# Performance work log

Hardware: AMD Instinct MI355X
Metric: run time of the kernel (lower is better)

The kernel has to match this reference:

```python
import jax, jax.numpy as jnp
import numpy as np

HEADS = 16
DIM_HEAD = 64
QUERY_DIM = 1024
CONTEXT_DIM = 1024
D_ATTN = HEADS * DIM_HEAD
SCALE = DIM_HEAD ** -0.5


def setup_inputs() -> dict:
    key = jax.random.key(0)
    ks = jax.random.split(key, 7)
    B, N, M = 4, 2048, 1024
    x = jax.random.normal(ks[0], (B, N, QUERY_DIM), dtype=jnp.float32)
    context = jax.random.normal(ks[1], (B, M, CONTEXT_DIM), dtype=jnp.float32)
    # Linear weights stored as [in, out] (no bias for Q/K/V, bias for to_out)
    s = 0.02
    Wq = jax.random.normal(ks[2], (QUERY_DIM, D_ATTN), dtype=jnp.float32) * s
    Wk = jax.random.normal(ks[3], (CONTEXT_DIM, D_ATTN), dtype=jnp.float32) * s
    Wv = jax.random.normal(ks[4], (CONTEXT_DIM, D_ATTN), dtype=jnp.float32) * s
    Wo = jax.random.normal(ks[5], (D_ATTN, QUERY_DIM), dtype=jnp.float32) * s
    bo = jax.random.normal(ks[6], (QUERY_DIM,), dtype=jnp.float32) * s
    return {"x": x, "context": context, "Wq": Wq, "Wk": Wk, "Wv": Wv, "Wo": Wo, "bo": bo}


def reference(x, context, Wq, Wk, Wv, Wo, bo):
    B, N, _ = x.shape
    M = context.shape[1]
    Q = (x @ Wq).reshape(B, N, HEADS, DIM_HEAD)        # b n h d
    K = (context @ Wk).reshape(B, M, HEADS, DIM_HEAD)  # b m h d
    V = (context @ Wv).reshape(B, M, HEADS, DIM_HEAD)
    # scores: b q h m  (matches torch einsum 'bqhd,bhmd->bqhm')
    scores = jnp.einsum('bqhd,bmhd->bqhm', Q, K) * SCALE
    attn = jax.nn.softmax(scores, axis=-1)
    out = jnp.einsum('bqhm,bmhd->bqhd', attn, V)
    out = out.reshape(B, N, D_ATTN)
    return out @ Wo + bo  # dropout p=0.0 -> identity
```

## Files before the change

### kernel.cpp

```cpp
#include <hip/hip_runtime.h>
#include <math.h>


#define HEADS 16
#define DHEAD 64
#define DM    1024
#define BQ    4
#define NQ    2048
#define MK    1024

typedef unsigned short u16;
typedef __attribute__((ext_vector_type(8))) short bf16x8;
typedef __attribute__((ext_vector_type(4))) float f32x4;
typedef __attribute__((ext_vector_type(16))) float f32x16;

__device__ __forceinline__ u16 f2bf(float f) {
  unsigned u = __builtin_bit_cast(unsigned, f);
  u = u + 0x7FFFu + ((u >> 16) & 1u);
  return (u16)(u >> 16);
}

__device__ __forceinline__ unsigned cvtpk(float lo, float hi2) {
  unsigned r;
  asm("v_cvt_pk_bf16_f32 %0, %1, %2" : "=v"(r) : "v"(lo), "v"(hi2));
  return r;
}

__device__ __forceinline__ float max3f(float a, float b, float c) {
  float d;
  asm("v_max3_f32 %0, %1, %2, %3" : "=v"(d) : "v"(a), "v"(b), "v"(c));
  return d;
}

__device__ __forceinline__ void gld16(const u16* g, u16* l) {
  __builtin_amdgcn_global_load_lds((const __attribute__((address_space(1))) void*)g,
                                   (__attribute__((address_space(3))) void*)l,
                                   16, 0, 0);
}

__global__ void k_cvt(const float* __restrict__ in, u16* __restrict__ out, int n8) {
  int i = blockIdx.x * 256 + threadIdx.x;
  if (i >= n8) return;
  float4 a = ((const float4*)in)[i * 2];
  float4 b = ((const float4*)in)[i * 2 + 1];
  union { u16 h[8]; int4 v; } r;
  r.h[0] = f2bf(a.x); r.h[1] = f2bf(a.y); r.h[2] = f2bf(a.z); r.h[3] = f2bf(a.w);
  r.h[4] = f2bf(b.x); r.h[5] = f2bf(b.y); r.h[6] = f2bf(b.z); r.h[7] = f2bf(b.w);
  ((int4*)out)[i] = r.v;
}

__global__ void k_wt(const float* __restrict__ W0, const float* __restrict__ W1,
                     const float* __restrict__ W2, const float* __restrict__ W3,
                     u16* __restrict__ out) {
  __shared__ float t[32][33];
  const float* W = blockIdx.z == 0 ? W0 : blockIdx.z == 1 ? W1 : blockIdx.z == 2 ? W2 : W3;
  u16* o = out + (size_t)blockIdx.z * DM * DM;
  int r0 = blockIdx.y * 32, c0 = blockIdx.x * 32;
  int tx = threadIdx.x, ty = threadIdx.y;
  for (int i = ty; i < 32; i += 8) t[i][tx] = W[(size_t)(r0 + i) * DM + c0 + tx];
  __syncthreads();
  for (int i = ty; i < 32; i += 8) o[(size_t)(c0 + i) * DM + r0 + tx] = f2bf(t[tx][i]);
}


#define VM6 asm volatile("s_waitcnt vmcnt(6)" ::: "memory")

#define STAGE_A8(bufi, h, kof) do {                                          \
  gld16(gA + (size_t)(h) * 131072 + (kof), &As8[bufi][(h) * 8192 + w * 512]); \
  gld16(gA + (size_t)(h) * 131072 + 65536 + (kof),                           \
        &As8[bufi][(h) * 8192 + 4096 + w * 512]);                            \
} while (0)

#define STAGE_B8(bufi, h, kof) do {                                          \
  gld16(gB + (size_t)(h) * 131072 + (kof), &Bs8[bufi][(h) * 8192 + w * 512]); \
  gld16(gB + (size_t)(h) * 131072 + 65536 + (kof),                           \
        &Bs8[bufi][(h) * 8192 + 4096 + w * 512]);                            \
} while (0)

#define RD_A8(qm) do { _Pragma("unroll")                                     \
  for (int mi = 0; mi < 4; ++mi) {                                           \
    const u16* pa = &As8[cur][((qm) * 128 + wmo + mi * 16 + lrow) * 64];     \
    af8[mi][0] = *(const bf16x8*)(pa + fo0);                                 \
    af8[mi][1] = *(const bf16x8*)(pa + (fo0 ^ 32));                          \
  } } while (0)

#define RD_B8(qn) do { _Pragma("unroll")                                     \
  for (int ni = 0; ni < 2; ++ni) {                                           \
    const u16* pb = &Bs8[cur][((qn) * 128 + wno + ni * 16 + lrow) * 64];     \
    bf8[ni][0] = *(const bf16x8*)(pb + fo0);                                 \
    bf8[ni][1] = *(const bf16x8*)(pb + (fo0 ^ 32));                          \
  } } while (0)

#define MM16(qm, qn) do {                                                    \
  __builtin_amdgcn_s_setprio(1);                                             \
  _Pragma("unroll")                                                          \
  for (int mi = 0; mi < 4; ++mi)                                             \
    _Pragma("unroll")                                                        \
    for (int ni = 0; ni < 2; ++ni) {                                         \
      acc[qm][qn][mi][ni] = __builtin_amdgcn_mfma_f32_16x16x32_bf16(         \
          af8[mi][0], bf8[ni][0], acc[qm][qn][mi][ni], 0, 0, 0);             \
      acc[qm][qn][mi][ni] = __builtin_amdgcn_mfma_f32_16x16x32_bf16(         \
          af8[mi][1], bf8[ni][1], acc[qm][qn][mi][ni], 0, 0, 0);             \
    }                                                                        \
  __builtin_amdgcn_s_setprio(0);                                             \
} while (0)

#define PH8(RDS, STG, VM, qm, qn) do {                                       \
  RDS;                                                                       \
  __builtin_amdgcn_sched_barrier(0);                                         \
  STG;                                                                       \
  VM;                                                                        \
  __builtin_amdgcn_s_barrier();                                              \
  asm volatile("s_waitcnt lgkmcnt(0)" ::: "memory");                         \
  __builtin_amdgcn_sched_barrier(0);                                         \
  MM16(qm, qn);                                                              \
  __builtin_amdgcn_sched_barrier(0);                                         \
  __builtin_amdgcn_s_barrier();                                              \
} while (0)

__global__ __launch_bounds__(512, 2) void k_gemm_qkv(const u16* __restrict__ xb,
                                                     const u16* __restrict__ cb,
                                                     const u16* __restrict__ wt,
                                                     u16* __restrict__ Qb,
                                                     u16* __restrict__ Kb,
                                                     u16* __restrict__ Vtb) {
  __shared__ u16 As8[2][16384];
  __shared__ u16 Bs8[2][16384];
  int lin = blockIdx.x;
  int swz = (lin & 7) * 32 + (lin >> 3);
  int p = swz >> 2, bx = swz & 3;
  const u16* A; const u16* Bt; u16* obf; int row0, mode;
  if (p < 32)      { A = xb; Bt = wt;           obf = Qb;  row0 = p * 256;        mode = 0; }
  else if (p < 48) { A = cb; Bt = wt + 1048576; obf = Kb;  row0 = (p - 32) * 256; mode = 0; }
  else             { A = cb; Bt = wt + 2097152; obf = Vtb; row0 = (p - 48) * 256; mode = 1; }
  int col0 = bx * 256;
  int t = threadIdx.x;
  int w = t >> 6, lane = t & 63, lrow = lane & 15, lgrp = lane >> 4;
  int wmo = (w >> 2) * 64, wno = (w & 3) * 32;
  int fo0 = (lgrp ^ (lrow & 7)) * 8;
  f32x4 acc[2][2][4][2] = {};
  bf16x8 af8[4][2], bf8[2][2];
  int srow = t >> 3, sunit = (t & 7) ^ ((t >> 3) & 7);
  const u16* gA = A  + (size_t)(row0 + srow) * DM + sunit * 8;
  const u16* gB = Bt + (size_t)(col0 + srow) * DM + sunit * 8;

  STAGE_A8(0, 0, 0);
  STAGE_B8(0, 1, 0);
  STAGE_B8(0, 0, 0);
  STAGE_A8(0, 1, 0);
  STAGE_A8(1, 0, 64);
  STAGE_B8(1, 1, 64);
  VM6;
  __syncthreads();

  #pragma unroll 2
  for (int u = 0; u < 16; ++u) {
    int cur = u & 1, nxt = cur ^ 1;
    int k1 = (u >= 15 ? 15 : u + 1) * 64;
    int k2 = (u >= 14 ? 15 : u + 2) * 64;
    PH8({ RD_A8(0); RD_B8(0); }, STAGE_B8(nxt, 0, k1), VM6,     0, 0);
    PH8({ RD_B8(1); },           STAGE_A8(nxt, 1, k1), (void)0, 0, 1);
    PH8({ RD_A8(1); },           STAGE_A8(cur, 0, k2), (void)0, 1, 1);
    PH8({ RD_B8(0); },           STAGE_B8(cur, 1, k2), VM6,     1, 0);
  }

  #pragma unroll
  for (int qm = 0; qm < 2; ++qm)
    #pragma unroll
    for (int qn = 0; qn < 2; ++qn)
      #pragma unroll
      for (int mi = 0; mi < 4; ++mi)
        #pragma unroll
        for (int ni = 0; ni < 2; ++ni)
          #pragma unroll
          for (int j = 0; j < 4; ++j) {
            int gr = row0 + qm * 128 + wmo + mi * 16 + lgrp * 4 + j;
            int gc = col0 + qn * 128 + wno + ni * 16 + lrow;
            float v = acc[qm][qn][mi][ni][j];
            if (mode == 0) {
              obf[(size_t)gr * DM + gc] = f2bf(v);
            } else {
              int b = gr >> 10, m = gr & 1023;
              obf[((size_t)(b * DM + gc)) * MK + m] = f2bf(v);
            }
          }
}

#define OSTG_A(bufi, h, kof) do {                                            \
  gld16(gA + (size_t)(h) * 131072 + (kof), &As8[bufi][(h) * 8192 + w * 512]); \
  gld16(gA + (size_t)(h) * 131072 + 65536 + (kof),                           \
        &As8[bufi][(h) * 8192 + 4096 + w * 512]);                            \
} while (0)

#define OSTG_B(bufi, h, kof)                                                 \
  gld16(gB + (size_t)(h) * 65536 + (kof), &Bs8[bufi][(h) * 4096 + w * 512])

#define ORD_A(qm) do { _Pragma("unroll")                                     \
  for (int mi = 0; mi < 2; ++mi) {                                           \
    const u16* pa = &As8[cur][((qm) * 128 + wmo + mi * 16 + lrow) * 64];     \
    af[mi][0] = *(const bf16x8*)(pa + fo0);                                  \
    af[mi][1] = *(const bf16x8*)(pa + (fo0 ^ 32));                           \
  } } while (0)

#define ORD_B(qn, dst) do { _Pragma("unroll")                                \
  for (int ni = 0; ni < 2; ++ni) {                                           \
    const u16* pb = &Bs8[cur][((qn) * 64 + wno + ni * 16 + lrow) * 64];      \
    dst[ni][0] = *(const bf16x8*)(pb + fo0);                                 \
    dst[ni][1] = *(const bf16x8*)(pb + (fo0 ^ 32));                          \
  } } while (0)

#define OMM(qm, qn, bfq) do {                                                \
  __builtin_amdgcn_s_setprio(1);                                             \
  _Pragma("unroll")                                                          \
  for (int mi = 0; mi < 2; ++mi)                                             \
    _Pragma("unroll")                                                        \
    for (int ni = 0; ni < 2; ++ni) {                                         \
      acc[qm][qn][mi][ni] = __builtin_amdgcn_mfma_f32_16x16x32_bf16(         \
          af[mi][0], bfq[ni][0], acc[qm][qn][mi][ni], 0, 0, 0);              \
      acc[qm][qn][mi][ni] = __builtin_amdgcn_mfma_f32_16x16x32_bf16(         \
          af[mi][1], bfq[ni][1], acc[qm][qn][mi][ni], 0, 0, 0);              \
    }                                                                        \
  __builtin_amdgcn_s_setprio(0);                                             \
} while (0)

#define OPH(RDS, STG, VM, qm, qn, bfq) do {                                  \
  RDS;                                                                       \
  __builtin_amdgcn_sched_barrier(0);                                         \
  STG;                                                                       \
  VM;                                                                        \
  __builtin_amdgcn_s_barrier();                                              \
  asm volatile("s_waitcnt lgkmcnt(0)" ::: "memory");                         \
  __builtin_amdgcn_sched_barrier(0);                                         \
  OMM(qm, qn, bfq);                                                          \
  __builtin_amdgcn_sched_barrier(0);                                         \
  __builtin_amdgcn_s_barrier();                                              \
} while (0)

__global__ __launch_bounds__(512, 2) void k_gemm_o(const u16* __restrict__ A,
                                                   const u16* __restrict__ Bt,
                                                   float* __restrict__ of32,
                                                   const float* __restrict__ bias) {
  __shared__ u16 As8[2][16384];
  __shared__ u16 Bs8[2][8192];
  int lin = blockIdx.x;
  int swz = (lin & 7) * 32 + (lin >> 3);
  int p = swz >> 3, bx = swz & 7;
  int row0 = p * 256, col0 = bx * 128;
  int t = threadIdx.x;
  int w = t >> 6, lane = t & 63, lrow = lane & 15, lgrp = lane >> 4;
  int wmo = (w >> 1) * 32, wno = (w & 1) * 32;
  int fo0 = (lgrp ^ (lrow & 7)) * 8;
  f32x4 acc[2][2][2][2] = {};
  bf16x8 af[2][2], bfA[2][2], bfB[2][2];
  int srow = t >> 3, sunit = (t & 7) ^ ((t >> 3) & 7);
  const u16* gA = A  + (size_t)(row0 + srow) * DM + sunit * 8;
  const u16* gB = Bt + (size_t)(col0 + srow) * DM + sunit * 8;

  OSTG_A(0, 0, 0);
  OSTG_B(0, 1, 0);
  OSTG_B(0, 0, 0);
  OSTG_A(0, 1, 0);
  OSTG_A(1, 0, 64);
  OSTG_B(1, 1, 64);
  asm volatile("s_waitcnt vmcnt(5)" ::: "memory");
  __syncthreads();

  #pragma unroll 2
  for (int u = 0; u < 16; ++u) {
    int cur = u & 1, nxt = cur ^ 1;
    int k1 = (u >= 15 ? 15 : u + 1) * 64;
    int k2 = (u >= 14 ? 15 : u + 2) * 64;
    OPH({ ORD_A(0); ORD_B(0, bfA); }, OSTG_B(nxt, 0, k1),
        asm volatile("s_waitcnt vmcnt(4)" ::: "memory"), 0, 0, bfA);
    OPH({ ORD_B(1, bfB); },           OSTG_A(nxt, 1, k1), (void)0, 0, 1, bfB);
    OPH({ ORD_A(1); },                OSTG_A(cur, 0, k2), (void)0, 1, 1, bfB);
    OPH({ (void)0; },                 OSTG_B(cur, 1, k2),
        asm volatile("s_waitcnt vmcnt(5)" ::: "memory"), 1, 0, bfA);
  }

  #pragma unroll
  for (int qm = 0; qm < 2; ++qm)
    #pragma unroll
    for (int qn = 0; qn < 2; ++qn)
      #pragma unroll
      for (int mi = 0; mi < 2; ++mi)
        #pragma unroll
        for (int ni = 0; ni < 2; ++ni)
          #pragma unroll
          for (int j = 0; j < 4; ++j) {
            int gr = row0 + qm * 128 + wmo + mi * 16 + lgrp * 4 + j;
            int gc = col0 + qn * 64 + wno + ni * 16 + lrow;
            of32[(size_t)gr * DM + gc] = acc[qm][qn][mi][ni][j] + bias[gc];
          }
}

#define BUILD_PFRAG(sv, base, frag) {                     \
  unsigned a_ = cvtpk(sv[base + 0], sv[base + 1]);        \
  unsigned c_ = cvtpk(sv[base + 2], sv[base + 3]);        \
  unsigned b_ = cvtpk(sv[base + 4], sv[base + 5]);        \
  unsigned d_ = cvtpk(sv[base + 6], sv[base + 7]);        \
  asm("v_permlane32_swap_b32 %0, %1" : "+v"(a_), "+v"(b_)); \
  asm("v_permlane32_swap_b32 %0, %1" : "+v"(c_), "+v"(d_)); \
  union { unsigned w[4]; bf16x8 v; } u_;                  \
  u_.w[0] = a_;  u_.w[1] = c_;                            \
  u_.w[2] = b_;  u_.w[3] = d_;                            \
  frag = u_.v; }

#define PV_CHUNK(sv, base, c) {                                               \
  bf16x8 pf_; BUILD_PFRAG(sv, base, pf_);                                     \
  int mo_ = ((c) * 16 + hi * 8) ^ sw;                                         \
  bf16x8 vf0_ = *(const bf16x8*)&Vl[cur][ln * 64 + mo_];                      \
  bf16x8 vf1_ = *(const bf16x8*)&Vl[cur][(32 + ln) * 64 + mo_];               \
  __builtin_amdgcn_s_setprio(1);                                              \
  o0 = __builtin_amdgcn_mfma_f32_32x32x16_bf16(vf0_, pf_, o0, 0, 0, 0);       \
  o1 = __builtin_amdgcn_mfma_f32_32x32x16_bf16(vf1_, pf_, o1, 0, 0, 0);       \
  __builtin_amdgcn_s_setprio(0); }

__device__ __forceinline__ float max16(const f32x16 &v) {
  float m0 = max3f(v[0], v[1], v[2]);
  float m1 = max3f(v[3], v[4], v[5]);
  float m2 = max3f(v[6], v[7], v[8]);
  float m3 = max3f(v[9], v[10], v[11]);
  float m4 = max3f(v[12], v[13], v[14]);
  float a = max3f(m0, m1, m2);
  float b = max3f(m3, m4, v[15]);
  return fmaxf(a, b);
}

__device__ __forceinline__ float sum16(const f32x16 &v) {
  float a = (v[0] + v[1]) + (v[2] + v[3]);
  float b = (v[4] + v[5]) + (v[6] + v[7]);
  float c = (v[8] + v[9]) + (v[10] + v[11]);
  float d = (v[12] + v[13]) + (v[14] + v[15]);
  return (a + b) + (c + d);
}

__global__ __launch_bounds__(512) void k_attn(const u16* __restrict__ Q,
                                              const u16* __restrict__ K,
                                              const u16* __restrict__ Vt,
                                              u16* __restrict__ O) {
  __shared__ __align__(16) u16 Kl[2][4096];
  __shared__ __align__(16) u16 Vl[2][4096];
  int wgid = blockIdx.x;
  int bh = (wgid & 7) * 8 + (wgid >> 6);
  int nt = (wgid >> 3) & 7;
  int b = bh >> 4, h = bh & 15;
  int n0 = nt * 256;
  int t = threadIdx.x, w = t >> 6, lane = t & 63;
  int ln = lane & 31, hi = lane >> 5;
  const float s2 = 0.18033688011112042f;

  int qrow = n0 + w * 32 + ln;
  const u16* qp = &Q[(((size_t)(b * NQ + qrow)) * HEADS + h) * DHEAD + hi * 8];
  bf16x8 qf0 = *(const bf16x8*)(qp);
  bf16x8 qf1 = *(const bf16x8*)(qp + 16);
  bf16x8 qf2 = *(const bf16x8*)(qp + 32);
  bf16x8 qf3 = *(const bf16x8*)(qp + 48);

  f32x16 o0 = {}, o1 = {};
  float M_ = -1e30f, L_ = 0.f;

  int srow = t >> 3, sp = (t & 7) * 8;
  const u16* kg = &K[(((size_t)(b * MK + srow)) * HEADS + h) * DHEAD + sp];
  const u16* vg = &Vt[((size_t)(b * DM) + h * DHEAD + srow) * MK + sp];
  int sd = srow * 64 + (sp ^ ((srow & 7) << 3));
  int sw = (ln & 7) << 3;

  int4 kv = *(const int4*)kg;
  int4 vv = *(const int4*)vg;
  *(int4*)&Kl[0][sd] = kv;
  *(int4*)&Vl[0][sd] = vv;
  __syncthreads();

  for (int it = 0; it < 16; ++it) {
    int cur = it & 1;
    if (it < 15) {
      kv = *(const int4*)(kg + (size_t)(it + 1) * (64 * HEADS * DHEAD));
      vv = *(const int4*)(vg + (it + 1) * 64);
    }

    f32x16 s0 = {}, s1 = {};
    __builtin_amdgcn_s_setprio(1);
    #pragma unroll
    for (int kd = 0; kd < 4; ++kd) {
      int doff = (kd * 16 + hi * 8) ^ sw;
      bf16x8 kf0 = *(const bf16x8*)&Kl[cur][ln * 64 + doff];
      bf16x8 kf1 = *(const bf16x8*)&Kl[cur][(32 + ln) * 64 + doff];
      bf16x8 qk = kd == 0 ? qf0 : kd == 1 ? qf1 : kd == 2 ? qf2 : qf3;
      s0 = __builtin_amdgcn_mfma_f32_32x32x16_bf16(kf0, qk, s0, 0, 0, 0);
      s1 = __builtin_amdgcn_mfma_f32_32x32x16_bf16(kf1, qk, s1, 0, 0, 0);
    }
    __builtin_amdgcn_s_setprio(0);

    float vm = fmaxf(max16(s0), max16(s1));

    if (!__all(vm - M_ <= 8.0f)) {
      float vm2 = fmaxf(vm, __shfl_xor(vm, 32));
      float mn = fmaxf(M_, vm2);
      float rc = exp2f((M_ - mn) * s2);
      M_ = mn;
      L_ *= rc;
      #pragma unroll
      for (int i = 0; i < 16; ++i) { o0[i] *= rc; o1[i] *= rc; }
    }
    float nb = M_ * s2;
    #pragma unroll
    for (int i = 0; i < 16; ++i) s0[i] = exp2f(s0[i] * s2 - nb);
    #pragma unroll
    for (int i = 0; i < 16; ++i) s1[i] = exp2f(s1[i] * s2 - nb);
    L_ += sum16(s0) + sum16(s1);

    PV_CHUNK(s0, 0, 0);
    PV_CHUNK(s0, 8, 1);
    PV_CHUNK(s1, 0, 2);
    PV_CHUNK(s1, 8, 3);

    if (it < 15) {
      *(int4*)&Kl[cur ^ 1][sd] = kv;
      *(int4*)&Vl[cur ^ 1][sd] = vv;
    }
    __syncthreads();
  }

  float Lt = L_ + __shfl_xor(L_, 32);
  float inv = 1.0f / Lt;
  u16* ob = (u16*)&O[(((size_t)(b * NQ + qrow)) * HEADS + h) * DHEAD];
  #pragma unroll
  for (int g = 0; g < 4; ++g) {
    union { u16 h4[4]; uint2 v; } r0, r1;
    #pragma unroll
    for (int s = 0; s < 4; ++s) {
      r0.h4[s] = f2bf(o0[4 * g + s] * inv);
      r1.h4[s] = f2bf(o1[4 * g + s] * inv);
    }
    *(uint2*)(ob + 8 * g + 4 * hi) = r0.v;
    *(uint2*)(ob + 32 + 8 * g + 4 * hi) = r1.v;
  }
}

extern "C" void kernel_launch(void* const* d_in, const int* in_sizes, int n_in,
                              void* d_out, int out_size, void* d_ws, size_t ws_size,
                              hipStream_t stream) {
  (void)in_sizes; (void)n_in; (void)out_size; (void)ws_size;
  const float* x   = (const float*)d_in[0];
  const float* ctx = (const float*)d_in[1];
  const float* Wq  = (const float*)d_in[2];
  const float* Wk  = (const float*)d_in[3];
  const float* Wv  = (const float*)d_in[4];
  const float* Wo  = (const float*)d_in[5];
  const float* bo  = (const float*)d_in[6];
  float* out = (float*)d_out;
  char* ws = (char*)d_ws;
  const size_t MB = 1u << 20;
  u16* xb  = (u16*)(ws);
  u16* cb  = (u16*)(ws + 16 * MB);
  u16* wt  = (u16*)(ws + 24 * MB);
  u16* Qb  = (u16*)(ws + 32 * MB);
  u16* Kb  = (u16*)(ws + 48 * MB);
  u16* Vtb = (u16*)(ws + 56 * MB);
  u16* Ab  = (u16*)(ws + 64 * MB);

  k_cvt<<<4096, 256, 0, stream>>>(x,   xb, 1048576);
  k_cvt<<<2048, 256, 0, stream>>>(ctx, cb, 524288);
  k_wt<<<dim3(32, 32, 4), dim3(32, 8), 0, stream>>>(Wq, Wk, Wv, Wo, wt);

  k_gemm_qkv<<<256, 512, 0, stream>>>(xb, cb, wt, Qb, Kb, Vtb);

  k_attn<<<512, 512, 0, stream>>>(Qb, Kb, Vtb, Ab);

  k_gemm_o<<<256, 512, 0, stream>>>(Ab, wt + 3145728, out, bo);
}
```

Before: 163.1 us.

## Fold softmax scale into Q projection and compute row sums with MFMA

The Q projection epilogue now multiplies by scale·log2(e), so the attention loop only subtracts the running max before a raw v_exp_f32, using packed f32 adds. The softmax denominator is no longer a VALU reduction; an extra MFMA per PV chunk multiplies P by a ones fragment, and the final shuffle combine goes away. The rescale of O is done with packed multiplies, and the lazy-rescale threshold is restated in the new scaled units. This trades VALU work in the softmax for more MFMA issue. Q is now rounded to bf16 after scaling, which slightly changes rounding.

```diff
diff --git a/kernel.cpp b/kernel.cpp
--- a/kernel.cpp
+++ b/kernel.cpp
@@ -11,6 +11,7 @@
 
 typedef unsigned short u16;
 typedef __attribute__((ext_vector_type(8))) short bf16x8;
+typedef __attribute__((ext_vector_type(2))) float f32x2;
 typedef __attribute__((ext_vector_type(4))) float f32x4;
 typedef __attribute__((ext_vector_type(16))) float f32x16;
 
@@ -29,6 +30,23 @@
 __device__ __forceinline__ float max3f(float a, float b, float c) {
   float d;
   asm("v_max3_f32 %0, %1, %2, %3" : "=v"(d) : "v"(a), "v"(b), "v"(c));
+  return d;
+}
+
+__device__ __forceinline__ float fexp2(float x) {
+  float r;
+  asm("v_exp_f32 %0, %1" : "=v"(r) : "v"(x));
+  return r;
+}
+
+__device__ __forceinline__ f32x2 pk_add(f32x2 a, f32x2 b) {
+  f32x2 d;
+  asm("v_pk_add_f32 %0, %1, %2" : "=v"(d) : "v"(a), "v"(b));
+  return d;
+}
+__device__ __forceinline__ f32x2 pk_mul(f32x2 a, f32x2 b) {
+  f32x2 d;
+  asm("v_pk_mul_f32 %0, %1, %2" : "=v"(d) : "v"(a), "v"(b));
   return d;
 }
 
@@ -130,9 +148,10 @@
   int swz = (lin & 7) * 32 + (lin >> 3);
   int p = swz >> 2, bx = swz & 3;
   const u16* A; const u16* Bt; u16* obf; int row0, mode;
-  if (p < 32)      { A = xb; Bt = wt;           obf = Qb;  row0 = p * 256;        mode = 0; }
-  else if (p < 48) { A = cb; Bt = wt + 1048576; obf = Kb;  row0 = (p - 32) * 256; mode = 0; }
-  else             { A = cb; Bt = wt + 2097152; obf = Vtb; row0 = (p - 48) * 256; mode = 1; }
+  float osc;
+  if (p < 32)      { A = xb; Bt = wt;           obf = Qb;  row0 = p * 256;        mode = 0; osc = 0.18033688011112042f; }
+  else if (p < 48) { A = cb; Bt = wt + 1048576; obf = Kb;  row0 = (p - 32) * 256; mode = 0; osc = 1.0f; }
+  else             { A = cb; Bt = wt + 2097152; obf = Vtb; row0 = (p - 48) * 256; mode = 1; osc = 1.0f; }
   int col0 = bx * 256;
   int t = threadIdx.x;
   int w = t >> 6, lane = t & 63, lrow = lane & 15, lgrp = lane >> 4;
@@ -176,7 +195,7 @@
           for (int j = 0; j < 4; ++j) {
             int gr = row0 + qm * 128 + wmo + mi * 16 + lgrp * 4 + j;
             int gc = col0 + qn * 128 + wno + ni * 16 + lrow;
-            float v = acc[qm][qn][mi][ni][j];
+            float v = acc[qm][qn][mi][ni][j] * osc;
             if (mode == 0) {
               obf[(size_t)gr * DM + gc] = f2bf(v);
             } else {
@@ -314,6 +333,7 @@
   __builtin_amdgcn_s_setprio(1);                                              \
   o0 = __builtin_amdgcn_mfma_f32_32x32x16_bf16(vf0_, pf_, o0, 0, 0, 0);       \
   o1 = __builtin_amdgcn_mfma_f32_32x32x16_bf16(vf1_, pf_, o1, 0, 0, 0);       \
+  Lacc = __builtin_amdgcn_mfma_f32_32x32x16_bf16(onesf, pf_, Lacc, 0, 0, 0);  \
   __builtin_amdgcn_s_setprio(0); }
 
 __device__ __forceinline__ float max16(const f32x16 &v) {
@@ -325,14 +345,6 @@
   float a = max3f(m0, m1, m2);
   float b = max3f(m3, m4, v[15]);
   return fmaxf(a, b);
-}
-
-__device__ __forceinline__ float sum16(const f32x16 &v) {
-  float a = (v[0] + v[1]) + (v[2] + v[3]);
-  float b = (v[4] + v[5]) + (v[6] + v[7]);
-  float c = (v[8] + v[9]) + (v[10] + v[11]);
-  float d = (v[12] + v[13]) + (v[14] + v[15]);
-  return (a + b) + (c + d);
 }
 
 __global__ __launch_bounds__(512) void k_attn(const u16* __restrict__ Q,
@@ -348,7 +360,6 @@
   int n0 = nt * 256;
   int t = threadIdx.x, w = t >> 6, lane = t & 63;
   int ln = lane & 31, hi = lane >> 5;
-  const float s2 = 0.18033688011112042f;
 
   int qrow = n0 + w * 32 + ln;
   const u16* qp = &Q[(((size_t)(b * NQ + qrow)) * HEADS + h) * DHEAD + hi * 8];
@@ -357,8 +368,11 @@
   bf16x8 qf2 = *(const bf16x8*)(qp + 32);
   bf16x8 qf3 = *(const bf16x8*)(qp + 48);
 
-  f32x16 o0 = {}, o1 = {};
-  float M_ = -1e30f, L_ = 0.f;
+  const short one_ = (short)0x3F80;
+  bf16x8 onesf = {one_, one_, one_, one_, one_, one_, one_, one_};
+
+  f32x16 o0 = {}, o1 = {}, Lacc = {};
+  float M_ = -1e30f;
 
   int srow = t >> 3, sp = (t & 7) * 8;
   const u16* kg = &K[(((size_t)(b * MK + srow)) * HEADS + h) * DHEAD + sp];
@@ -394,21 +408,31 @@
 
     float vm = fmaxf(max16(s0), max16(s1));
 
-    if (!__all(vm - M_ <= 8.0f)) {
+    if (!__all(vm - M_ <= 1.44269504f)) {
       float vm2 = fmaxf(vm, __shfl_xor(vm, 32));
       float mn = fmaxf(M_, vm2);
-      float rc = exp2f((M_ - mn) * s2);
+      float rc = fexp2(M_ - mn);
       M_ = mn;
-      L_ *= rc;
+      Lacc[0] *= rc;
+      f32x2 rc2 = {rc, rc};
+      f32x2* o0p = (f32x2*)&o0;
+      f32x2* o1p = (f32x2*)&o1;
       #pragma unroll
-      for (int i = 0; i < 16; ++i) { o0[i] *= rc; o1[i] *= rc; }
+      for (int i = 0; i < 8; ++i) { o0p[i] = pk_mul(o0p[i], rc2); }
+      #pragma unroll
+      for (int i = 0; i < 8; ++i) { o1p[i] = pk_mul(o1p[i], rc2); }
     }
-    float nb = M_ * s2;
-    #pragma unroll
-    for (int i = 0; i < 16; ++i) s0[i] = exp2f(s0[i] * s2 - nb);
-    #pragma unroll
-    for (int i = 0; i < 16; ++i) s1[i] = exp2f(s1[i] * s2 - nb);
-    L_ += sum16(s0) + sum16(s1);
+    f32x2 nb2 = {-M_, -M_};
+    f32x2* s0p = (f32x2*)&s0;
+    f32x2* s1p = (f32x2*)&s1;
+    #pragma unroll
+    for (int i = 0; i < 8; ++i) s0p[i] = pk_add(s0p[i], nb2);
+    #pragma unroll
+    for (int i = 0; i < 8; ++i) s1p[i] = pk_add(s1p[i], nb2);
+    #pragma unroll
+    for (int i = 0; i < 16; ++i) s0[i] = fexp2(s0[i]);
+    #pragma unroll
+    for (int i = 0; i < 16; ++i) s1[i] = fexp2(s1[i]);
 
     PV_CHUNK(s0, 0, 0);
     PV_CHUNK(s0, 8, 1);
@@ -422,8 +446,7 @@
     __syncthreads();
   }
 
-  float Lt = L_ + __shfl_xor(L_, 32);
-  float inv = 1.0f / Lt;
+  float inv = 1.0f / Lacc[0];
   u16* ob = (u16*)&O[(((size_t)(b * NQ + qrow)) * HEADS + h) * DHEAD];
   #pragma unroll
   for (int g = 0; g < 4; ++g) {
```

Measured after the change: 155.5 us. -4.7%, faster.
